# Kernel tuning notes

Hardware: AMD Instinct MI355X
Metric: run time of the kernel (lower is better)

## Reference

```python
import jax, jax.numpy as jnp
import numpy as np

K = 16
H = 128

def _gelu(x):
    return jax.nn.gelu(x, approximate=False)  # torch nn.GELU default (erf)

def _knn_idx(xyz, k):
    # squared pairwise distances; topk of squared dist == topk of cdist (monotone)
    sq = jnp.sum(xyz * xyz, axis=-1)  # [B,N]
    d2 = sq[:, :, None] + sq[:, None, :] - 2.0 * jnp.einsum('bnd,bmd->bnm', xyz, xyz)
    n = xyz.shape[1]
    d2 = d2.at[:, jnp.arange(n), jnp.arange(n)].set(-1.0)  # force self first
    _, idx = jax.lax.top_k(-d2, min(k + 1, n))  # smallest distances
    return idx[..., 1:]  # drop self -> [B,N,K]

def _gather(feat, idx):
    # feat [B,N,C], idx [B,N,K] -> [B,N,K,C]
    return jax.vmap(lambda f, i: f[i])(feat, idx)

def setup_inputs() -> dict:
    key = jax.random.key(0)
    ks = jax.random.split(key, 13)
    s = 0.05
    return {
        'points': jax.random.normal(ks[0], (4, 4096, 6), jnp.float32),
        'Wc1': jax.random.normal(ks[1], (3, H), jnp.float32) * s,
        'bc1': jnp.zeros((H,), jnp.float32),
        'Wc2': jax.random.normal(ks[2], (H, H), jnp.float32) * s,
        'bc2': jnp.zeros((H,), jnp.float32),
        'Wn1': jax.random.normal(ks[3], (4, H), jnp.float32) * s,
        'bn1': jnp.zeros((H,), jnp.float32),
        'Wn2': jax.random.normal(ks[4], (H, H), jnp.float32) * s,
        'bn2': jnp.zeros((H,), jnp.float32),
        'Wo1': jax.random.normal(ks[5], (2 * H, H), jnp.float32) * s,
        'bo1': jnp.zeros((H,), jnp.float32),
        'Wo2': jax.random.normal(ks[6], (H, H), jnp.float32) * s,
        'bo2': jnp.zeros((H,), jnp.float32),
        'k': K,
    }

def reference(points, Wc1, bc1, Wc2, bc2, Wn1, bn1, Wn2, bn2, Wo1, bo1, Wo2, bo2, k):
    xyz = points[..., :3]
    normals = points[..., 3:6]
    idx = jax.lax.stop_gradient(_knn_idx(xyz, k))  # [B,N,K]

    # coord branch: relative neighbor coords -> MLP -> max over K
    rel_xyz = _gather(xyz, idx) - xyz[:, :, None, :]          # [B,N,K,3]
    h = _gelu(rel_xyz @ Wc1 + bc1) @ Wc2 + bc2                # [B,N,K,H]
    coord_feat = jnp.max(h, axis=2)                           # [B,N,H]

    # normal branch: neighbor normals + 1 - cos variation
    neigh_n = _gather(normals, idx)                           # [B,N,K,3]
    variation = 1.0 - jnp.sum(normals[:, :, None, :] * neigh_n, axis=-1, keepdims=True)
    nin = jnp.concatenate([neigh_n, variation], axis=-1)      # [B,N,K,4]
    g = _gelu(nin @ Wn1 + bn1) @ Wn2 + bn2                    # [B,N,K,H]
    normal_feat = jnp.max(g, axis=2)                          # [B,N,H]

    cat = jnp.concatenate([coord_feat, normal_feat], axis=-1) # [B,N,2H]
    return _gelu(cat @ Wo1 + bo1) @ Wo2 + bo2                 # [B,N,H]
```

## Files before the change

kernel.cpp:

```cpp
#include <hip/hip_runtime.h>
#include <math.h>

#define BATCH 4
#define NPTS 4096
#define KNBR 16
#define HDIM 128

typedef __attribute__((ext_vector_type(8))) short bf16x8;
typedef __attribute__((ext_vector_type(4))) float f32x4;
typedef unsigned long long u64;

#define WSOFF_W (1u << 20)
#define WC_HI 0
#define WC_LO 16384
#define WN_HI 32768
#define WN_LO 49152
#define WO1_HI 65536
#define WO1_LO 98304
#define WO2_HI 131072
#define WO2_LO 147456

__device__ __forceinline__ float gelu_f(float x) {
    const float z = x * 0.7071067811865476f;
    const float u = fabsf(z);
    const float z2 = z * z;
    const float t = __builtin_amdgcn_rcpf(fmaf(0.3275911f, u, 1.0f));
    const float E = __expf(-z2);
    float p = fmaf(t, 1.061405429f, -1.453152027f);
    p = fmaf(t, p, 1.421413741f);
    p = fmaf(t, p, -0.284496736f);
    p = fmaf(t, p, 0.254829592f);
    p = p * t;
    const float e = fmaf(-p, E, 1.0f);
    const float hx = 0.5f * x;
    return fmaf(fabsf(hx), e, hx);
}

__device__ __forceinline__ void bsplit(float x, short& hi, short& lo) {
    const unsigned u = __float_as_uint(x);
    hi = (short)(u >> 16);
    const float r = x - __uint_as_float(u & 0xffff0000u);
    lo = (short)(__float_as_uint(r) >> 16);
}

__device__ __forceinline__ u64 readlane_u64(u64 v, int src) {
    const unsigned lo = (unsigned)__builtin_amdgcn_readlane((int)(unsigned)v, src);
    const unsigned hi = (unsigned)__builtin_amdgcn_readlane((int)(unsigned)(v >> 32), src);
    return ((u64)hi << 32) | lo;
}

__global__ __launch_bounds__(256) void prep_points(const float* __restrict__ pts,
                                                   float4* __restrict__ ctab) {
    const int e = blockIdx.x * 256 + threadIdx.x;
    const float* __restrict__ p = pts + (size_t)e * 6;
    const float x = p[0], y = p[1], z = p[2];
    const float sq = x * x + y * y + z * z;
    ctab[e] = make_float4(x, y, z, sq);
}

__global__ __launch_bounds__(256) void prep_weights(
    const float* __restrict__ Wc2, const float* __restrict__ Wn2,
    const float* __restrict__ Wo1, const float* __restrict__ Wo2,
    unsigned short* __restrict__ wbuf)
{
    const int e = blockIdx.x * 256 + threadIdx.x;
    const float* src;
    unsigned short *dh, *dl;
    int idx;
    if (e < 16384)      { src = Wc2; dh = wbuf + WC_HI;  dl = wbuf + WC_LO;  idx = e; }
    else if (e < 32768) { src = Wn2; dh = wbuf + WN_HI;  dl = wbuf + WN_LO;  idx = e - 16384; }
    else if (e < 65536) { src = Wo1; dh = wbuf + WO1_HI; dl = wbuf + WO1_LO; idx = e - 32768; }
    else                { src = Wo2; dh = wbuf + WO2_HI; dl = wbuf + WO2_LO; idx = e - 65536; }
    const int j = idx & 7;
    const int l = (idx >> 3) & 63;
    const int tile = idx >> 9;
    const int ct = tile & 7;
    const int ks = tile >> 3;
    const int n = (l & 15) + 16 * ct;
    const int k = ks * 32 + ((l >> 4) << 3) + j;
    const float x = src[k * 128 + n];
    short hi, lo;
    bsplit(x, hi, lo);
    dh[idx] = (unsigned short)hi;
    dl[idx] = (unsigned short)lo;
}

__global__ __launch_bounds__(256) void knn_kernel(const float4* __restrict__ ctab,
                                                  int* __restrict__ idx_out) {
    const int wq = blockIdx.x * 4 + (threadIdx.x >> 6);
    const int b = wq >> 12;
    const int n = wq & (NPTS - 1);
    const int lane = threadIdx.x & 63;
    const float4* __restrict__ cb = ctab + (size_t)b * NPTS;

    const float4 q = cb[n];

    u64 run = ~0ull;
    u64 cur16max = ~0ull;

    for (int c = 0; c < NPTS / 64; ++c) {
        const int m = lane + 64 * c;
        const float4 cc = cb[m];
        const float dot = q.x * cc.x + q.y * cc.y + q.z * cc.z;
        float d2 = (q.w + cc.w) - 2.0f * dot;
        d2 = fmaxf(d2, 0.0f);
        u64 key = ((u64)__float_as_uint(d2) << 32) | (unsigned)m;
        if (m == n) key = ~0ull;

        u64 mask = __ballot(key < cur16max);
        while (mask) {
            const int src = (int)__builtin_ctzll(mask);
            const u64 K = readlane_u64(key, src);
            u64 prev = __shfl_up(run, 1, 64);
            if (lane == 0) prev = 0;
            run = (run < K) ? run : ((prev < K) ? K : prev);
            cur16max = readlane_u64(run, 15);
            mask &= mask - 1;
            mask &= __ballot(key < cur16max);
        }
    }

    if (lane < KNBR)
        idx_out[((size_t)b * NPTS + n) * KNBR + lane] = (int)(run & 0xffffffffull);
}

template<int NIN>
__device__ __forceinline__ void branch_compute(
    const float (* __restrict__ inp)[4],
    const float* __restrict__ W1,
    const float* __restrict__ b1,
    const float* __restrict__ b2,
    const unsigned short* __restrict__ w2hi,
    const unsigned short* __restrict__ w2lo,
    unsigned short (* __restrict__ catH)[264],
    unsigned short (* __restrict__ catL)[264],
    int colbase, int w, int l)
{
    const int lr = l & 15;
    const int lq = l >> 4;
    const int kb = lq * 8;

    f32x4 acc[2][8];
#pragma unroll
    for (int rt = 0; rt < 2; ++rt)
#pragma unroll
        for (int ct = 0; ct < 8; ++ct)
            acc[rt][ct] = (f32x4){0.f, 0.f, 0.f, 0.f};

    for (int ks = 0; ks < 4; ++ks) {
        const int c0 = ks * 32 + kb;
        bf16x8 bh[8], bl[8];
        const unsigned short* fb = w2hi + ((size_t)(ks * 8) * 64 + l) * 8;
        const unsigned short* fq = w2lo + ((size_t)(ks * 8) * 64 + l) * 8;
#pragma unroll
        for (int ct = 0; ct < 8; ++ct) {
            bh[ct] = *(const bf16x8*)(fb + ct * 512);
            bl[ct] = *(const bf16x8*)(fq + ct * 512);
        }
        float wr[NIN][8], bb[8];
#pragma unroll
        for (int d = 0; d < NIN; ++d) {
            *(float4*)&wr[d][0] = *(const float4*)(W1 + (d << 7) + c0);
            *(float4*)&wr[d][4] = *(const float4*)(W1 + (d << 7) + c0 + 4);
        }
        *(float4*)&bb[0] = *(const float4*)(b1 + c0);
        *(float4*)&bb[4] = *(const float4*)(b1 + c0 + 4);

        bf16x8 ah[2], al[2];
#pragma unroll
        for (int rt = 0; rt < 2; ++rt) {
            const int row = 32 * w + 16 * rt + lr;
            const float4 rv = *(const float4*)&inp[row][0];
#pragma unroll
            for (int jj = 0; jj < 8; ++jj) {
                float x = bb[jj] + rv.x * wr[0][jj] + rv.y * wr[1][jj] + rv.z * wr[2][jj];
                if (NIN == 4) x += rv.w * wr[3][jj];
                x = gelu_f(x);
                short hi, lo;
                bsplit(x, hi, lo);
                ah[rt][jj] = hi;
                al[rt][jj] = lo;
            }
        }
#pragma unroll
        for (int ct = 0; ct < 8; ++ct) {
#pragma unroll
            for (int rt = 0; rt < 2; ++rt) {
                acc[rt][ct] = __builtin_amdgcn_mfma_f32_16x16x32_bf16(ah[rt], bh[ct], acc[rt][ct], 0, 0, 0);
                acc[rt][ct] = __builtin_amdgcn_mfma_f32_16x16x32_bf16(ah[rt], bl[ct], acc[rt][ct], 0, 0, 0);
                acc[rt][ct] = __builtin_amdgcn_mfma_f32_16x16x32_bf16(al[rt], bh[ct], acc[rt][ct], 0, 0, 0);
            }
        }
    }
#pragma unroll
    for (int rt = 0; rt < 2; ++rt) {
        const int p = 2 * w + rt;
#pragma unroll
        for (int ct = 0; ct < 8; ++ct) {
            const f32x4 a = acc[rt][ct];
            float m = fmaxf(fmaxf(a[0], a[1]), fmaxf(a[2], a[3]));
            m = fmaxf(m, __shfl_xor(m, 16));
            m = fmaxf(m, __shfl_xor(m, 32));
            const int col = lr + 16 * ct;
            const float v = m + b2[col];
            if (lq == 0) {
                short hi, lo;
                bsplit(v, hi, lo);
                catH[p][colbase + col] = (unsigned short)hi;
                catL[p][colbase + col] = (unsigned short)lo;
            }
        }
    }
}

__global__ __launch_bounds__(256, 3) void mlp_mfma(
    const float* __restrict__ pts, const int* __restrict__ knn_idx,
    const float* __restrict__ Wc1, const float* __restrict__ bc1,
    const float* __restrict__ bc2,
    const float* __restrict__ Wn1, const float* __restrict__ bn1,
    const float* __restrict__ bn2,
    const float* __restrict__ bo1, const float* __restrict__ bo2,
    const unsigned short* __restrict__ wbuf,
    float* __restrict__ outp)
{
    __shared__ __align__(16) float rel[128][4];
    __shared__ __align__(16) float nin[128][4];
    __shared__ float qpt[8][6];
    __shared__ __align__(16) unsigned short catH[8][264];
    __shared__ __align__(16) unsigned short catL[8][264];
    __shared__ __align__(16) unsigned short o1H[8][136];
    __shared__ __align__(16) unsigned short o1L[8][136];

    const int t = threadIdx.x;
    const int w = t >> 6;
    const int l = t & 63;
    const int lr = l & 15;
    const int lq = l >> 4;
    const int kb = lq * 8;
    const int blk = blockIdx.x;
    const int b = blk >> 9;
    const int n0 = (blk & 511) * 8;
    const float* __restrict__ base = pts + (size_t)b * NPTS * 6;

    if (t < 48) qpt[t / 6][t % 6] = base[(size_t)(n0 + t / 6) * 6 + (t % 6)];
    __syncthreads();
    if (t < 128) {
        const int p = t >> 4;
        const int m = knn_idx[((size_t)b * NPTS + n0 + p) * KNBR + (t & 15)];
        const float cx = base[(size_t)m * 6 + 0];
        const float cy = base[(size_t)m * 6 + 1];
        const float cz = base[(size_t)m * 6 + 2];
        const float nx = base[(size_t)m * 6 + 3];
        const float ny = base[(size_t)m * 6 + 4];
        const float nz = base[(size_t)m * 6 + 5];
        rel[t][0] = cx - qpt[p][0];
        rel[t][1] = cy - qpt[p][1];
        rel[t][2] = cz - qpt[p][2];
        rel[t][3] = 0.0f;
        nin[t][0] = nx; nin[t][1] = ny; nin[t][2] = nz;
        nin[t][3] = 1.0f - (qpt[p][3] * nx + qpt[p][4] * ny + qpt[p][5] * nz);
    }
    __syncthreads();

    branch_compute<3>(rel, Wc1, bc1, bc2, wbuf + WC_HI, wbuf + WC_LO,
                      catH, catL, 0, w, l);
    branch_compute<4>(nin, Wn1, bn1, bn2, wbuf + WN_HI, wbuf + WN_LO,
                      catH, catL, 128, w, l);
    __syncthreads();

    {
        f32x4 a1[2];
        a1[0] = (f32x4){0.f, 0.f, 0.f, 0.f};
        a1[1] = (f32x4){0.f, 0.f, 0.f, 0.f};
#pragma unroll
        for (int ks = 0; ks < 8; ++ks) {
            const int c0 = ks * 32 + kb;
            const bf16x8 ah = *(const bf16x8*)&catH[lr & 7][c0];
            const bf16x8 al = *(const bf16x8*)&catL[lr & 7][c0];
#pragma unroll
            for (int c2 = 0; c2 < 2; ++c2) {
                const int ct = 2 * w + c2;
                const unsigned short* wp = wbuf + WO1_HI + ((size_t)((ks * 8 + ct) * 64 + l)) * 8;
                const bf16x8 bh = *(const bf16x8*)wp;
                const bf16x8 bl = *(const bf16x8*)(wp + (WO1_LO - WO1_HI));
                a1[c2] = __builtin_amdgcn_mfma_f32_16x16x32_bf16(ah, bh, a1[c2], 0, 0, 0);
                a1[c2] = __builtin_amdgcn_mfma_f32_16x16x32_bf16(ah, bl, a1[c2], 0, 0, 0);
                a1[c2] = __builtin_amdgcn_mfma_f32_16x16x32_bf16(al, bh, a1[c2], 0, 0, 0);
            }
        }
#pragma unroll
        for (int c2 = 0; c2 < 2; ++c2) {
            const int col = lr + 16 * (2 * w + c2);
            const float bo = bo1[col];
#pragma unroll
            for (int r = 0; r < 4; ++r) {
                const int prow = lq * 4 + r;
                if (prow < 8) {
                    const float x = gelu_f(a1[c2][r] + bo);
                    short hi, lo;
                    bsplit(x, hi, lo);
                    o1H[prow][col] = (unsigned short)hi;
                    o1L[prow][col] = (unsigned short)lo;
                }
            }
        }
    }
    __syncthreads();
    {
        f32x4 a2[2];
        a2[0] = (f32x4){0.f, 0.f, 0.f, 0.f};
        a2[1] = (f32x4){0.f, 0.f, 0.f, 0.f};
#pragma unroll
        for (int ks = 0; ks < 4; ++ks) {
            const int c0 = ks * 32 + kb;
            const bf16x8 ah = *(const bf16x8*)&o1H[lr & 7][c0];
            const bf16x8 al = *(const bf16x8*)&o1L[lr & 7][c0];
#pragma unroll
            for (int c2 = 0; c2 < 2; ++c2) {
                const int ct = 2 * w + c2;
                const unsigned short* wp = wbuf + WO2_HI + ((size_t)((ks * 8 + ct) * 64 + l)) * 8;
                const bf16x8 bh = *(const bf16x8*)wp;
                const bf16x8 bl = *(const bf16x8*)(wp + (WO2_LO - WO2_HI));
                a2[c2] = __builtin_amdgcn_mfma_f32_16x16x32_bf16(ah, bh, a2[c2], 0, 0, 0);
                a2[c2] = __builtin_amdgcn_mfma_f32_16x16x32_bf16(ah, bl, a2[c2], 0, 0, 0);
                a2[c2] = __builtin_amdgcn_mfma_f32_16x16x32_bf16(al, bh, a2[c2], 0, 0, 0);
            }
        }
#pragma unroll
        for (int c2 = 0; c2 < 2; ++c2) {
            const int col = lr + 16 * (2 * w + c2);
            const float bo = bo2[col];
#pragma unroll
            for (int r = 0; r < 4; ++r) {
                const int prow = lq * 4 + r;
                if (prow < 8)
                    outp[((size_t)b * NPTS + n0 + prow) * HDIM + col] = a2[c2][r] + bo;
            }
        }
    }
}

extern "C" void kernel_launch(void* const* d_in, const int* in_sizes, int n_in,
                              void* d_out, int out_size, void* d_ws, size_t ws_size,
                              hipStream_t stream) {
    const float* pts = (const float*)d_in[0];
    const float* Wc1 = (const float*)d_in[1];
    const float* bc1 = (const float*)d_in[2];
    const float* Wc2 = (const float*)d_in[3];
    const float* bc2 = (const float*)d_in[4];
    const float* Wn1 = (const float*)d_in[5];
    const float* bn1 = (const float*)d_in[6];
    const float* Wn2 = (const float*)d_in[7];
    const float* bn2 = (const float*)d_in[8];
    const float* Wo1 = (const float*)d_in[9];
    const float* bo1 = (const float*)d_in[10];
    const float* Wo2 = (const float*)d_in[11];
    const float* bo2 = (const float*)d_in[12];
    float* outp = (float*)d_out;
    int* idx = (int*)d_ws;
    float4* ctab = (float4*)((char*)d_ws + WSOFF_W);
    unsigned short* wbuf = (unsigned short*)((char*)d_ws + WSOFF_W);

    prep_points<<<dim3(BATCH * NPTS / 256), dim3(256), 0, stream>>>(pts, ctab);
    knn_kernel<<<dim3(BATCH * NPTS / 4), dim3(256), 0, stream>>>(ctab, idx);
    prep_weights<<<dim3(320), dim3(256), 0, stream>>>(Wc2, Wn2, Wo1, Wo2, wbuf);
    mlp_mfma<<<dim3(BATCH * NPTS / 8), dim3(256), 0, stream>>>(
        pts, idx, Wc1, bc1, bc2, Wn1, bn1, bn2, bo1, bo2, wbuf, outp);
}
```

Baseline: 190.2 us.

## Restructure branch MLP loop order, stage small weights in LDS, raise occupancy

The branch computation now builds all GELU activation fragments first, then loops over output column tiles with only two accumulators live, loading second-layer weight fragments per column tile instead of holding 16 B fragments and 16 accumulators at once. First-layer weights and all biases are copied into shared memory at block start. Launch bounds go from 3 to 4 blocks per SIMD-level hint to cut register pressure and raise occupancy. In exchange, activation fragments for all four K-slices are held in registers, and the LDS footprint grows a little.

```diff
diff --git a/kernel.cpp b/kernel.cpp
--- a/kernel.cpp
+++ b/kernel.cpp
@@ -127,9 +127,9 @@
 template<int NIN>
 __device__ __forceinline__ void branch_compute(
     const float (* __restrict__ inp)[4],
-    const float* __restrict__ W1,
-    const float* __restrict__ b1,
-    const float* __restrict__ b2,
+    const float* __restrict__ w1s,
+    const float* __restrict__ b1s,
+    const float* __restrict__ b2s,
     const unsigned short* __restrict__ w2hi,
     const unsigned short* __restrict__ w2lo,
     unsigned short (* __restrict__ catH)[264],
@@ -140,33 +140,18 @@
     const int lq = l >> 4;
     const int kb = lq * 8;
 
-    f32x4 acc[2][8];
-#pragma unroll
-    for (int rt = 0; rt < 2; ++rt)
-#pragma unroll
-        for (int ct = 0; ct < 8; ++ct)
-            acc[rt][ct] = (f32x4){0.f, 0.f, 0.f, 0.f};
-
+    bf16x8 ah[4][2], al[4][2];
+#pragma unroll
     for (int ks = 0; ks < 4; ++ks) {
         const int c0 = ks * 32 + kb;
-        bf16x8 bh[8], bl[8];
-        const unsigned short* fb = w2hi + ((size_t)(ks * 8) * 64 + l) * 8;
-        const unsigned short* fq = w2lo + ((size_t)(ks * 8) * 64 + l) * 8;
-#pragma unroll
-        for (int ct = 0; ct < 8; ++ct) {
-            bh[ct] = *(const bf16x8*)(fb + ct * 512);
-            bl[ct] = *(const bf16x8*)(fq + ct * 512);
-        }
         float wr[NIN][8], bb[8];
 #pragma unroll
         for (int d = 0; d < NIN; ++d) {
-            *(float4*)&wr[d][0] = *(const float4*)(W1 + (d << 7) + c0);
-            *(float4*)&wr[d][4] = *(const float4*)(W1 + (d << 7) + c0 + 4);
-        }
-        *(float4*)&bb[0] = *(const float4*)(b1 + c0);
-        *(float4*)&bb[4] = *(const float4*)(b1 + c0 + 4);
-
-        bf16x8 ah[2], al[2];
+            *(float4*)&wr[d][0] = *(const float4*)(w1s + (d << 7) + c0);
+            *(float4*)&wr[d][4] = *(const float4*)(w1s + (d << 7) + c0 + 4);
+        }
+        *(float4*)&bb[0] = *(const float4*)(b1s + c0);
+        *(float4*)&bb[4] = *(const float4*)(b1s + c0 + 4);
 #pragma unroll
         for (int rt = 0; rt < 2; ++rt) {
             const int row = 32 * w + 16 * rt + lr;
@@ -178,31 +163,38 @@
                 x = gelu_f(x);
                 short hi, lo;
                 bsplit(x, hi, lo);
-                ah[rt][jj] = hi;
-                al[rt][jj] = lo;
-            }
-        }
-#pragma unroll
-        for (int ct = 0; ct < 8; ++ct) {
+                ah[ks][rt][jj] = hi;
+                al[ks][rt][jj] = lo;
+            }
+        }
+    }
+
+#pragma unroll
+    for (int ct = 0; ct < 8; ++ct) {
+        f32x4 acc[2];
+        acc[0] = (f32x4){0.f, 0.f, 0.f, 0.f};
+        acc[1] = (f32x4){0.f, 0.f, 0.f, 0.f};
+#pragma unroll
+        for (int ks = 0; ks < 4; ++ks) {
+            const size_t off = ((size_t)((ks * 8 + ct) * 64 + l)) * 8;
+            const bf16x8 bh = *(const bf16x8*)(w2hi + off);
+            const bf16x8 bl = *(const bf16x8*)(w2lo + off);
 #pragma unroll
             for (int rt = 0; rt < 2; ++rt) {
-                acc[rt][ct] = __builtin_amdgcn_mfma_f32_16x16x32_bf16(ah[rt], bh[ct], acc[rt][ct], 0, 0, 0);
-                acc[rt][ct] = __builtin_amdgcn_mfma_f32_16x16x32_bf16(ah[rt], bl[ct], acc[rt][ct], 0, 0, 0);
-                acc[rt][ct] = __builtin_amdgcn_mfma_f32_16x16x32_bf16(al[rt], bh[ct], acc[rt][ct], 0, 0, 0);
-            }
-        }
-    }
-#pragma unroll
-    for (int rt = 0; rt < 2; ++rt) {
-        const int p = 2 * w + rt;
-#pragma unroll
-        for (int ct = 0; ct < 8; ++ct) {
-            const f32x4 a = acc[rt][ct];
+                acc[rt] = __builtin_amdgcn_mfma_f32_16x16x32_bf16(ah[ks][rt], bh, acc[rt], 0, 0, 0);
+                acc[rt] = __builtin_amdgcn_mfma_f32_16x16x32_bf16(ah[ks][rt], bl, acc[rt], 0, 0, 0);
+                acc[rt] = __builtin_amdgcn_mfma_f32_16x16x32_bf16(al[ks][rt], bh, acc[rt], 0, 0, 0);
+            }
+        }
+#pragma unroll
+        for (int rt = 0; rt < 2; ++rt) {
+            const int p = 2 * w + rt;
+            const f32x4 a = acc[rt];
             float m = fmaxf(fmaxf(a[0], a[1]), fmaxf(a[2], a[3]));
             m = fmaxf(m, __shfl_xor(m, 16));
             m = fmaxf(m, __shfl_xor(m, 32));
             const int col = lr + 16 * ct;
-            const float v = m + b2[col];
+            const float v = m + b2s[col];
             if (lq == 0) {
                 short hi, lo;
                 bsplit(v, hi, lo);
@@ -213,7 +205,7 @@
     }
 }
 
-__global__ __launch_bounds__(256, 3) void mlp_mfma(
+__global__ __launch_bounds__(256, 4) void mlp_mfma(
     const float* __restrict__ pts, const int* __restrict__ knn_idx,
     const float* __restrict__ Wc1, const float* __restrict__ bc1,
     const float* __restrict__ bc2,
@@ -230,6 +222,9 @@
     __shared__ __align__(16) unsigned short catL[8][264];
     __shared__ __align__(16) unsigned short o1H[8][136];
     __shared__ __align__(16) unsigned short o1L[8][136];
+    __shared__ __align__(16) float w1c[3 * 128];
+    __shared__ __align__(16) float w1n[4 * 128];
+    __shared__ __align__(16) float b1c[128], b2c[128], b1n[128], b2n[128], bo1s[128], bo2s[128];
 
     const int t = threadIdx.x;
     const int w = t >> 6;
@@ -242,6 +237,13 @@
     const int n0 = (blk & 511) * 8;
     const float* __restrict__ base = pts + (size_t)b * NPTS * 6;
 
+    for (int i = t; i < 384; i += 256) w1c[i] = Wc1[i];
+    for (int i = t; i < 512; i += 256) w1n[i] = Wn1[i];
+    if (t < 128) {
+        b1c[t] = bc1[t]; b2c[t] = bc2[t];
+        b1n[t] = bn1[t]; b2n[t] = bn2[t];
+        bo1s[t] = bo1[t]; bo2s[t] = bo2[t];
+    }
     if (t < 48) qpt[t / 6][t % 6] = base[(size_t)(n0 + t / 6) * 6 + (t % 6)];
     __syncthreads();
     if (t < 128) {
@@ -262,9 +264,9 @@
     }
     __syncthreads();
 
-    branch_compute<3>(rel, Wc1, bc1, bc2, wbuf + WC_HI, wbuf + WC_LO,
+    branch_compute<3>(rel, w1c, b1c, b2c, wbuf + WC_HI, wbuf + WC_LO,
                       catH, catL, 0, w, l);
-    branch_compute<4>(nin, Wn1, bn1, bn2, wbuf + WN_HI, wbuf + WN_LO,
+    branch_compute<4>(nin, w1n, b1n, b2n, wbuf + WN_HI, wbuf + WN_LO,
                       catH, catL, 128, w, l);
     __syncthreads();
 
@@ -291,7 +293,7 @@
 #pragma unroll
         for (int c2 = 0; c2 < 2; ++c2) {
             const int col = lr + 16 * (2 * w + c2);
-            const float bo = bo1[col];
+            const float bo = bo1s[col];
 #pragma unroll
             for (int r = 0; r < 4; ++r) {
                 const int prow = lq * 4 + r;
@@ -329,7 +331,7 @@
 #pragma unroll
         for (int c2 = 0; c2 < 2; ++c2) {
             const int col = lr + 16 * (2 * w + c2);
-            const float bo = bo2[col];
+            const float bo = bo2s[col];
 #pragma unroll
             for (int r = 0; r < 4; ++r) {
                 const int prow = lq * 4 + r;
```

Result: slower. 203.1 us (+6.8%).
